# Kernel optimization log

Measured on AMD Instinct MI355X. Metric: run time of the kernel, lower is better.

The kernel has to match this reference:

```python
import jax, jax.numpy as jnp
import numpy as np

B, T, D_MEM, D_Q, D_ATT, C_LOC, K = 64, 2000, 512, 1024, 128, 32, 31


def setup_inputs() -> dict:
    key = jax.random.key(0)
    ks = jax.random.split(key, 9)
    return {
        "attention_hidden_state": jax.random.normal(ks[0], (B, 1, D_Q), jnp.float32),
        "memory": jax.random.normal(ks[1], (B, T, D_MEM), jnp.float32),
        "processed_memory": jax.random.normal(ks[2], (B, T, D_ATT), jnp.float32),
        "attention_weights": jax.random.uniform(ks[3], (B, 2, T), jnp.float32),
        "Wq": jax.random.normal(ks[4], (D_Q, D_ATT), jnp.float32) * 0.02,
        "Wconv": jax.random.normal(ks[5], (C_LOC, 2, K), jnp.float32) * 0.1,
        "bconv": jax.random.normal(ks[6], (C_LOC,), jnp.float32) * 0.01,
        "Wloc": jax.random.normal(ks[7], (C_LOC, D_ATT), jnp.float32) * 0.1,
        "v": jax.random.normal(ks[8], (D_ATT,), jnp.float32) * 0.1,
    }


def reference(attention_hidden_state, memory, processed_memory, attention_weights,
              Wq, Wconv, bconv, Wloc, v):
    # query projection: [B,1,1024] @ [1024,128] -> [B,1,128]
    processed_query = jnp.einsum("bqi,io->bqo", attention_hidden_state, Wq)
    # location conv: [B,2,T] -> [B,32,T], 'same' padding (k=31, pad=15)
    loc = jax.lax.conv_general_dilated(
        attention_weights, Wconv, window_strides=(1,), padding=[(15, 15)],
        dimension_numbers=("NCH", "OIH", "NCH"))
    loc = loc + bconv[None, :, None]
    # transpose to [B,T,32] then project to [B,T,128]
    processed_loc = jnp.einsum("bct,co->bto", loc, Wloc)
    # energies: v . tanh(q + loc + mem) -> [B,T]
    energies = jnp.einsum("btd,d->bt", jnp.tanh(processed_query + processed_loc + processed_memory), v)
    new_weights = jax.nn.softmax(energies, axis=1)
    # context: [B,T] x [B,T,D] -> [B,D]
    attention_context = jnp.einsum("bt,btd->bd", new_weights, memory)
    return attention_context, new_weights
```

## Files before the change

### kernel.cpp

```cpp
#include <hip/hip_runtime.h>
#include <hip/hip_bf16.h>

#define B 64
#define T 2000
#define D_MEM 512
#define D_Q 1024
#define D_ATT 128
#define C_LOC 32
#define K 31

#define CH2 100
#define NCH2 (T / CH2)
#define TPG 13
#define NPART (NCH2 * 2)

#define WS_PQ    0
#define WS_EXPW  (WS_PQ + B * D_ATT)
#define WS_SUMS  (WS_EXPW + B * T)
#define WS_PART  (WS_SUMS + B * NCH2)

__device__ __forceinline__ float tanh_fast(float x) {
    float e = __expf(2.f * x);
    return 1.f - 2.f / (e + 1.f);
}

__global__ __launch_bounds__(512) void pq_kernel(const float* __restrict__ h,
                                                 const float* __restrict__ Wq,
                                                 float* __restrict__ pq) {
    int b = blockIdx.x;
    int tid = threadIdx.x;
    int ty = tid >> 7;
    int d  = tid & 127;
    __shared__ float sh[D_Q];
    __shared__ float red[4][D_ATT];
    const float* hb = h + (size_t)b * D_Q;
    if (tid < D_Q / 4) ((float4*)sh)[tid] = ((const float4*)hb)[tid];
    __syncthreads();
    float acc = 0.f;
    int ibeg = ty * 256;
#pragma unroll 8
    for (int i2 = 0; i2 < 256; ++i2) {
        int i = ibeg + i2;
        acc = fmaf(sh[i], Wq[(size_t)i * D_ATT + d], acc);
    }
    red[ty][d] = acc;
    __syncthreads();
    if (ty == 0)
        pq[b * D_ATT + d] = red[0][d] + red[1][d] + red[2][d] + red[3][d];
}

__global__ __launch_bounds__(256, 4) void mega_kernel(
    const float* __restrict__ aw, const float* __restrict__ pmem,
    const float* __restrict__ pq, const float* __restrict__ Wconv,
    const float* __restrict__ bconv, const float* __restrict__ Wloc,
    const float* __restrict__ v, const float* __restrict__ memory,
    float* __restrict__ expw, float* __restrict__ sums,
    float* __restrict__ partial) {
    const int s = blockIdx.x, b = blockIdx.y;
    const int t0 = s * CH2;
    const int tid = threadIdx.x;

    __shared__ float s_aw[2][CH2 + K - 1];
    __shared__ float s_wc[2 * K * C_LOC];
    __shared__ float s_loc[128][C_LOC];
    __shared__ float s_wloc[C_LOC * D_ATT];
    __shared__ float s_pq[D_ATT];
    __shared__ float s_e[CH2];
    __shared__ float s_red[2];

    const int AWW = CH2 + K - 1;
    for (int j = tid; j < 2 * AWW; j += 256) {
        int i = j / AWW, o = j - i * AWW;
        int t = t0 - (K / 2) + o;
        s_aw[i][o] = (t >= 0 && t < T) ? aw[((size_t)b * 2 + i) * T + t] : 0.f;
    }
    for (int j = tid; j < C_LOC * 2 * K; j += 256) {
        int c = j / (2 * K), r = j - c * 2 * K;
        int i = r / K, k = r - i * K;
        s_wc[(i * K + k) * C_LOC + c] = Wconv[j];
    }
    for (int j = tid; j < C_LOC * D_ATT / 4; j += 256)
        ((float4*)s_wloc)[j] = ((const float4*)Wloc)[j];
    if (tid < D_ATT) s_pq[tid] = pq[b * D_ATT + tid];
    __syncthreads();

    {
        int g = tid >> 5, c = tid & 31;
        float bc = bconv[c];
        float acc[TPG];
#pragma unroll
        for (int j = 0; j < TPG; ++j) acc[j] = bc;
#pragma unroll
        for (int i = 0; i < 2; ++i) {
#pragma unroll
            for (int k = 0; k < K; ++k) {
                float wv = s_wc[(i * K + k) * C_LOC + c];
#pragma unroll
                for (int j = 0; j < TPG; ++j)
                    acc[j] = fmaf(s_aw[i][g + 8 * j + k], wv, acc[j]);
            }
        }
#pragma unroll
        for (int j = 0; j < TPG; ++j) s_loc[g + 8 * j][c] = acc[j];
    }
    __syncthreads();

    {
        int g = tid >> 5, dd = tid & 31;
        float4 pqv = ((const float4*)s_pq)[dd];
        float4 vv  = ((const float4*)v)[dd];
#pragma unroll
        for (int jc = 0; jc < 4; ++jc) {
            float4 pl[4];
#pragma unroll
            for (int jj = 0; jj < 4; ++jj) pl[jj] = make_float4(0.f, 0.f, 0.f, 0.f);
#pragma unroll
            for (int c = 0; c < C_LOC; ++c) {
                float4 w = ((const float4*)s_wloc)[c * (D_ATT / 4) + dd];
#pragma unroll
                for (int jj = 0; jj < 4; ++jj) {
                    float l = s_loc[g + 8 * (jc * 4 + jj)][c];
                    pl[jj].x = fmaf(l, w.x, pl[jj].x);
                    pl[jj].y = fmaf(l, w.y, pl[jj].y);
                    pl[jj].z = fmaf(l, w.z, pl[jj].z);
                    pl[jj].w = fmaf(l, w.w, pl[jj].w);
                }
            }
#pragma unroll
            for (int jj = 0; jj < 4; ++jj) {
                int tl = g + 8 * (jc * 4 + jj);
                if (tl < CH2) {
                    int t = t0 + tl;
                    float4 pm = ((const float4*)(pmem + ((size_t)b * T + t) * D_ATT))[dd];
                    float e = vv.x * tanh_fast(pqv.x + pl[jj].x + pm.x)
                            + vv.y * tanh_fast(pqv.y + pl[jj].y + pm.y)
                            + vv.z * tanh_fast(pqv.z + pl[jj].z + pm.z)
                            + vv.w * tanh_fast(pqv.w + pl[jj].w + pm.w);
#pragma unroll
                    for (int off = 16; off >= 1; off >>= 1)
                        e += __shfl_xor(e, off);
                    if (dd == 0) s_e[tl] = __expf(e);
                }
            }
        }
    }
    __syncthreads();

    if (tid < 128) {
        float vsum = (tid < CH2) ? s_e[tid] : 0.f;
        if (tid < CH2) expw[(size_t)b * T + t0 + tid] = vsum;
        float r = vsum;
#pragma unroll
        for (int off = 32; off >= 1; off >>= 1) r += __shfl_xor(r, off);
        if ((tid & 63) == 0) s_red[tid >> 6] = r;
    }
    __syncthreads();
    if (tid == 0) sums[b * NCH2 + s] = s_red[0] + s_red[1];

    {
        int dq = tid & 127, h = tid >> 7;
        const float4* mem4 =
            (const float4*)(memory + ((size_t)b * T + t0 + h * 50) * D_MEM);
        float4 acc = {0.f, 0.f, 0.f, 0.f};
#pragma unroll 10
        for (int j = 0; j < 50; ++j) {
            float wt = s_e[h * 50 + j];
            float4 mv = mem4[(size_t)j * (D_MEM / 4) + dq];
            acc.x = fmaf(wt, mv.x, acc.x);
            acc.y = fmaf(wt, mv.y, acc.y);
            acc.z = fmaf(wt, mv.z, acc.z);
            acc.w = fmaf(wt, mv.w, acc.w);
        }
        ((float4*)(partial + ((size_t)(s * 2 + h) * B + b) * D_MEM))[dq] = acc;
    }
}

__global__ __launch_bounds__(256) void finalize_kernel(
    const float* __restrict__ expw, const float* __restrict__ sums,
    const float* __restrict__ partial, float* __restrict__ out_w,
    float* __restrict__ out_ctx) {
    int b = blockIdx.x, tid = threadIdx.x;
    __shared__ float s_inv;
    if (tid < 64) {
        float r = (tid < NCH2) ? sums[b * NCH2 + tid] : 0.f;
#pragma unroll
        for (int off = 32; off >= 1; off >>= 1) r += __shfl_xor(r, off);
        if (tid == 0) s_inv = 1.f / r;
    }
    __syncthreads();
    float inv = s_inv;
    for (int t = tid; t < T; t += 256)
        out_w[(size_t)b * T + t] = expw[(size_t)b * T + t] * inv;
    if (tid < 128) {
        const float4* p4 = (const float4*)partial;
        float4 acc = {0.f, 0.f, 0.f, 0.f};
#pragma unroll
        for (int p = 0; p < NPART; ++p) {
            float4 pv = p4[((size_t)p * B + b) * (D_MEM / 4) + tid];
            acc.x += pv.x; acc.y += pv.y; acc.z += pv.z; acc.w += pv.w;
        }
        acc.x *= inv; acc.y *= inv; acc.z *= inv; acc.w *= inv;
        ((float4*)(out_ctx + (size_t)b * D_MEM))[tid] = acc;
    }
}

extern "C" void kernel_launch(void* const* d_in, const int* in_sizes, int n_in,
                              void* d_out, int out_size, void* d_ws, size_t ws_size,
                              hipStream_t stream) {
    const float* hidden = (const float*)d_in[0];
    const float* memory = (const float*)d_in[1];
    const float* pmem   = (const float*)d_in[2];
    const float* aw     = (const float*)d_in[3];
    const float* Wq     = (const float*)d_in[4];
    const float* Wconv  = (const float*)d_in[5];
    const float* bconv  = (const float*)d_in[6];
    const float* Wloc   = (const float*)d_in[7];
    const float* v      = (const float*)d_in[8];

    float* out_ctx = (float*)d_out;
    float* out_w   = (float*)d_out + B * D_MEM;

    float* ws      = (float*)d_ws;
    float* pqp     = ws + WS_PQ;
    float* expw    = ws + WS_EXPW;
    float* sums    = ws + WS_SUMS;
    float* partial = ws + WS_PART;

    pq_kernel<<<B, 512, 0, stream>>>(hidden, Wq, pqp);
    mega_kernel<<<dim3(NCH2, B), 256, 0, stream>>>(aw, pmem, pqp, Wconv, bconv,
                                                   Wloc, v, memory, expw, sums,
                                                   partial);
    finalize_kernel<<<B, 256, 0, stream>>>(expw, sums, partial, out_w, out_ctx);
}
```

Measured before the change: 461.8 us.

## Split context reduction into separate kernel and prefetch pmem before loc projection

```diff
diff --git a/kernel.cpp b/kernel.cpp
--- a/kernel.cpp
+++ b/kernel.cpp
@@ -1,5 +1,4 @@
 #include <hip/hip_runtime.h>
-#include <hip/hip_bf16.h>
 
 #define B 64
 #define T 2000
@@ -12,7 +11,8 @@
 #define CH2 100
 #define NCH2 (T / CH2)
 #define TPG 13
-#define NPART (NCH2 * 2)
+#define CH3 50
+#define NPART (T / CH3)
 
 #define WS_PQ    0
 #define WS_EXPW  (WS_PQ + B * D_ATT)
@@ -49,20 +49,19 @@
         pq[b * D_ATT + d] = red[0][d] + red[1][d] + red[2][d] + red[3][d];
 }
 
-__global__ __launch_bounds__(256, 4) void mega_kernel(
+__global__ __launch_bounds__(256, 4) void energy_kernel(
     const float* __restrict__ aw, const float* __restrict__ pmem,
     const float* __restrict__ pq, const float* __restrict__ Wconv,
     const float* __restrict__ bconv, const float* __restrict__ Wloc,
-    const float* __restrict__ v, const float* __restrict__ memory,
-    float* __restrict__ expw, float* __restrict__ sums,
-    float* __restrict__ partial) {
+    const float* __restrict__ v, float* __restrict__ expw,
+    float* __restrict__ sums) {
     const int s = blockIdx.x, b = blockIdx.y;
     const int t0 = s * CH2;
     const int tid = threadIdx.x;
 
     __shared__ float s_aw[2][CH2 + K - 1];
     __shared__ float s_wc[2 * K * C_LOC];
-    __shared__ float s_loc[128][C_LOC];
+    __shared__ float s_loc[104][C_LOC];
     __shared__ float s_wloc[C_LOC * D_ATT];
     __shared__ float s_pq[D_ATT];
     __shared__ float s_e[CH2];
@@ -111,14 +110,21 @@
         float4 vv  = ((const float4*)v)[dd];
 #pragma unroll
         for (int jc = 0; jc < 4; ++jc) {
-            float4 pl[4];
-#pragma unroll
-            for (int jj = 0; jj < 4; ++jj) pl[jj] = make_float4(0.f, 0.f, 0.f, 0.f);
+            const int NJ = (jc == 3) ? 1 : 4;
+            float4 pm[4], pl[4];
+#pragma unroll
+            for (int jj = 0; jj < NJ; ++jj) {
+                int tl = g + 8 * (jc * 4 + jj);
+                if (tl < CH2)
+                    pm[jj] = ((const float4*)(pmem +
+                              ((size_t)b * T + t0 + tl) * D_ATT))[dd];
+                pl[jj] = make_float4(0.f, 0.f, 0.f, 0.f);
+            }
 #pragma unroll
             for (int c = 0; c < C_LOC; ++c) {
                 float4 w = ((const float4*)s_wloc)[c * (D_ATT / 4) + dd];
 #pragma unroll
-                for (int jj = 0; jj < 4; ++jj) {
+                for (int jj = 0; jj < NJ; ++jj) {
                     float l = s_loc[g + 8 * (jc * 4 + jj)][c];
                     pl[jj].x = fmaf(l, w.x, pl[jj].x);
                     pl[jj].y = fmaf(l, w.y, pl[jj].y);
@@ -127,15 +133,13 @@
                 }
             }
 #pragma unroll
-            for (int jj = 0; jj < 4; ++jj) {
+            for (int jj = 0; jj < NJ; ++jj) {
                 int tl = g + 8 * (jc * 4 + jj);
                 if (tl < CH2) {
-                    int t = t0 + tl;
-                    float4 pm = ((const float4*)(pmem + ((size_t)b * T + t) * D_ATT))[dd];
-                    float e = vv.x * tanh_fast(pqv.x + pl[jj].x + pm.x)
-                            + vv.y * tanh_fast(pqv.y + pl[jj].y + pm.y)
-                            + vv.z * tanh_fast(pqv.z + pl[jj].z + pm.z)
-                            + vv.w * tanh_fast(pqv.w + pl[jj].w + pm.w);
+                    float e = vv.x * tanh_fast(pqv.x + pl[jj].x + pm[jj].x)
+                            + vv.y * tanh_fast(pqv.y + pl[jj].y + pm[jj].y)
+                            + vv.z * tanh_fast(pqv.z + pl[jj].z + pm[jj].z)
+                            + vv.w * tanh_fast(pqv.w + pl[jj].w + pm[jj].w);
 #pragma unroll
                     for (int off = 16; off >= 1; off >>= 1)
                         e += __shfl_xor(e, off);
@@ -156,28 +160,43 @@
     }
     __syncthreads();
     if (tid == 0) sums[b * NCH2 + s] = s_red[0] + s_red[1];
-
-    {
-        int dq = tid & 127, h = tid >> 7;
-        const float4* mem4 =
-            (const float4*)(memory + ((size_t)b * T + t0 + h * 50) * D_MEM);
-        float4 acc = {0.f, 0.f, 0.f, 0.f};
+}
+
+__global__ __launch_bounds__(128, 4) void ctx_kernel(
+    const float* __restrict__ expw, const float* __restrict__ sums,
+    const float* __restrict__ memory, float* __restrict__ partial,
+    float* __restrict__ out_w) {
+    const int p = blockIdx.x, b = blockIdx.y;
+    const int t0 = p * CH3;
+    const int tid = threadIdx.x;
+    __shared__ float s_w[CH3];
+    __shared__ float s_inv;
+    if (tid < 64) {
+        float r = (tid < NCH2) ? sums[b * NCH2 + tid] : 0.f;
+#pragma unroll
+        for (int off = 32; off >= 1; off >>= 1) r += __shfl_xor(r, off);
+        if (tid == 0) s_inv = 1.f / r;
+    }
+    if (tid < CH3) s_w[tid] = expw[(size_t)b * T + t0 + tid];
+    __syncthreads();
+    if (tid < CH3) out_w[(size_t)b * T + t0 + tid] = s_w[tid] * s_inv;
+
+    const float4* mem4 = (const float4*)(memory + ((size_t)b * T + t0) * D_MEM);
+    float4 acc = {0.f, 0.f, 0.f, 0.f};
 #pragma unroll 10
-        for (int j = 0; j < 50; ++j) {
-            float wt = s_e[h * 50 + j];
-            float4 mv = mem4[(size_t)j * (D_MEM / 4) + dq];
-            acc.x = fmaf(wt, mv.x, acc.x);
-            acc.y = fmaf(wt, mv.y, acc.y);
-            acc.z = fmaf(wt, mv.z, acc.z);
-            acc.w = fmaf(wt, mv.w, acc.w);
-        }
-        ((float4*)(partial + ((size_t)(s * 2 + h) * B + b) * D_MEM))[dq] = acc;
-    }
-}
-
-__global__ __launch_bounds__(256) void finalize_kernel(
-    const float* __restrict__ expw, const float* __restrict__ sums,
-    const float* __restrict__ partial, float* __restrict__ out_w,
+    for (int j = 0; j < CH3; ++j) {
+        float wt = s_w[j];
+        float4 mv = mem4[(size_t)j * (D_MEM / 4) + tid];
+        acc.x = fmaf(wt, mv.x, acc.x);
+        acc.y = fmaf(wt, mv.y, acc.y);
+        acc.z = fmaf(wt, mv.z, acc.z);
+        acc.w = fmaf(wt, mv.w, acc.w);
+    }
+    ((float4*)(partial + ((size_t)p * B + b) * D_MEM))[tid] = acc;
+}
+
+__global__ __launch_bounds__(128) void finalize_kernel(
+    const float* __restrict__ sums, const float* __restrict__ partial,
     float* __restrict__ out_ctx) {
     int b = blockIdx.x, tid = threadIdx.x;
     __shared__ float s_inv;
@@ -189,19 +208,15 @@
     }
     __syncthreads();
     float inv = s_inv;
-    for (int t = tid; t < T; t += 256)
-        out_w[(size_t)b * T + t] = expw[(size_t)b * T + t] * inv;
-    if (tid < 128) {
-        const float4* p4 = (const float4*)partial;
-        float4 acc = {0.f, 0.f, 0.f, 0.f};
-#pragma unroll
-        for (int p = 0; p < NPART; ++p) {
-            float4 pv = p4[((size_t)p * B + b) * (D_MEM / 4) + tid];
-            acc.x += pv.x; acc.y += pv.y; acc.z += pv.z; acc.w += pv.w;
-        }
-        acc.x *= inv; acc.y *= inv; acc.z *= inv; acc.w *= inv;
-        ((float4*)(out_ctx + (size_t)b * D_MEM))[tid] = acc;
-    }
+    const float4* p4 = (const float4*)partial;
+    float4 acc = {0.f, 0.f, 0.f, 0.f};
+#pragma unroll
+    for (int p = 0; p < NPART; ++p) {
+        float4 pv = p4[((size_t)p * B + b) * (D_MEM / 4) + tid];
+        acc.x += pv.x; acc.y += pv.y; acc.z += pv.z; acc.w += pv.w;
+    }
+    acc.x *= inv; acc.y *= inv; acc.z *= inv; acc.w *= inv;
+    ((float4*)(out_ctx + (size_t)b * D_MEM))[tid] = acc;
 }
 
 extern "C" void kernel_launch(void* const* d_in, const int* in_sizes, int n_in,
@@ -227,8 +242,9 @@
     float* partial = ws + WS_PART;
 
     pq_kernel<<<B, 512, 0, stream>>>(hidden, Wq, pqp);
-    mega_kernel<<<dim3(NCH2, B), 256, 0, stream>>>(aw, pmem, pqp, Wconv, bconv,
-                                                   Wloc, v, memory, expw, sums,
-                                                   partial);
-    finalize_kernel<<<B, 256, 0, stream>>>(expw, sums, partial, out_w, out_ctx);
-}
+    energy_kernel<<<dim3(NCH2, B), 256, 0, stream>>>(aw, pmem, pqp, Wconv,
+                                                     bconv, Wloc, v, expw, sums);
+    ctx_kernel<<<dim3(NPART, B), 128, 0, stream>>>(expw, sums, memory, partial,
+                                                   out_w);
+    finalize_kernel<<<B, 128, 0, stream>>>(sums, partial, out_ctx);
+}
```

Result: slower. 774.9 us (+67.8%).
